# Performance work log

Hardware: AMD Instinct MI355X
Metric: run time of the kernel (lower is better)

Reference implementation:

```python
import jax, jax.numpy as jnp
import numpy as np

N_LOC, N_EVT, E = 100000, 200000, 1000000
F_LOC, F_EVT, H = 128, 128, 64


def setup_inputs() -> dict:
    key = jax.random.key(0)
    ks = jax.random.split(key, 12)
    s = lambda k, shp: jax.random.normal(k, shp, dtype=jnp.float32) * (1.0 / np.sqrt(shp[0]))
    return {
        "loc_x": jax.random.normal(ks[0], (N_LOC, F_LOC), dtype=jnp.float32),
        "evt_x": jax.random.normal(ks[1], (N_EVT, F_EVT), dtype=jnp.float32),
        "edge_index": jax.random.randint(ks[2], (2, E), 0, N_LOC, dtype=jnp.int64),
        # projections (stored as (in, out))
        "W_loc": s(ks[3], (F_LOC, H)), "b_loc": jnp.zeros((H,), jnp.float32),
        "W_evt": s(ks[4], (F_EVT, H)), "b_evt": jnp.zeros((H,), jnp.float32),
        # SAGEConv: lin_l (on aggregated src, with bias), lin_r (on dst root, no bias)
        "W_l": s(ks[5], (H, H)), "b_l": jnp.zeros((H,), jnp.float32),
        "W_r": s(ks[6], (H, H)),
        # head MLP
        "W_h1": s(ks[7], (H, H // 2)), "b_h1": jnp.zeros((H // 2,), jnp.float32),
        "W_h2": s(ks[8], (H // 2, 1)), "b_h2": jnp.zeros((1,), jnp.float32),
    }


def reference(loc_x, evt_x, edge_index, W_loc, b_loc, W_evt, b_evt,
              W_l, b_l, W_r, W_h1, b_h1, W_h2, b_h2):
    # node projections + ReLU
    loc_h = jax.nn.relu(loc_x @ W_loc + b_loc)   # [N_loc, H]
    evt_h = jax.nn.relu(evt_x @ W_evt + b_evt)   # [N_evt, H]

    src, dst = edge_index[0], edge_index[1]      # event -> location
    n_loc = loc_h.shape[0]
    # mean aggregation of source (event) features onto destination (location) nodes
    msg_sum = jax.ops.segment_sum(evt_h[src], dst, num_segments=n_loc)   # [N_loc, H]
    cnt = jax.ops.segment_sum(jnp.ones_like(dst, dtype=loc_h.dtype), dst,
                              num_segments=n_loc)
    agg = msg_sum / jnp.maximum(cnt, 1.0)[:, None]
    # SAGEConv: lin_l(agg) + lin_r(root), then ReLU
    loc_h = jax.nn.relu(agg @ W_l + b_l + loc_h @ W_r)

    # prediction head
    h = jax.nn.relu(loc_h @ W_h1 + b_h1)
    logits = (h @ W_h2 + b_h2)[:, 0]             # [N_loc]
    return logits
```

## Files before the change

### kernel.cpp

```cpp
#include <hip/hip_runtime.h>


#define N_LOC 100000
#define N_EVT 200000
#define E_CNT 1000000
#define NTILES 6250
#define NBKT   256
#define BKT_L  391
#define CAPG   6000
#define QCAP   32
#define BKT_BLK 512
#define PERB   1954

#define PROJ_EVT_BLK 512
#define PROJ_LOC_BLK 256
#define PROJ_BLK_TOT (PROJ_EVT_BLK + PROJ_LOC_BLK)
#define EVT_TILES 12500
#define LOC_TILES 6250
#define HEAD_BLK  512

typedef __attribute__((ext_vector_type(8))) short short8;
typedef __attribute__((ext_vector_type(4))) float floatx4;

__device__ __forceinline__ float b2f(unsigned short u) {
    unsigned int x = ((unsigned int)u) << 16;
    return __builtin_bit_cast(float, x);
}
__device__ __forceinline__ unsigned short f2b(float f) {
    unsigned int x = __builtin_bit_cast(unsigned int, f);
    unsigned int r = (x + 0x7fffu + ((x >> 16) & 1u)) >> 16;
    return (unsigned short)r;
}
__device__ __forceinline__ float loadf(const void* p, int f32, size_t i) {
    return f32 ? ((const float*)p)[i] : b2f(((const unsigned short*)p)[i]);
}

__global__ __launch_bounds__(256) void prep_kernel(
    const void* t0, const void* t1, const int* eidx,
    const void* t3, const void* t4, const void* t5, const void* t6,
    const void* t7, const void* t8, const void* t9, const void* t10,
    const void* t11, const void* t12, const void* t13,
    int* flags, int* gbc, unsigned short* __restrict__ wp_all) {
    int b = blockIdx.x, tid = threadIdx.x;
    __shared__ int s0, s1;

    if (b == 14) { gbc[tid] = 0; return; }

    if (b >= 15) {
        int pb = b - 15;
        const void* W; int K, N, bstart, off;
        if (pb < 4)       { W = t5;  K = 128; N = 64; bstart = 0;  off = 0; }
        else if (pb < 8)  { W = t3;  K = 128; N = 64; bstart = 4;  off = 8192; }
        else if (pb < 10) { W = t7;  K = 64;  N = 64; bstart = 8;  off = 16384; }
        else if (pb < 12) { W = t9;  K = 64;  N = 64; bstart = 10; off = 20480; }
        else              { W = t10; K = 64;  N = 32; bstart = 12; off = 24576; }
        if (tid == 0) s0 = 0;
        __syncthreads();
        int nsamp = 2 * K * N; if (nsamp > 1024) nsamp = 1024;
        const unsigned short* h = (const unsigned short*)W;
        int susp = 0;
        for (int i = tid; i < nsamp; i += 256)
            if (((h[i] >> 7) & 0xFF) >= 0x90) susp++;
        if (susp) atomicAdd(&s0, susp);
        __syncthreads();
        int f32 = (s0 * 16 >= nsamp) ? 1 : 0;

        int idx  = (pb - bstart) * 256 + tid;
        int nk   = K >> 5;
        int f    = idx >> 6;
        int lane = idx & 63;
        int t  = f / nk;
        int kk = f - t * nk;
        int n  = t * 16 + (lane & 15);
        int k0 = kk * 32 + (lane >> 4) * 8;
        unsigned short tmp[8];
#pragma unroll
        for (int j = 0; j < 8; ++j) {
            size_t src = (size_t)(k0 + j) * N + n;
            tmp[j] = f32 ? f2b(((const float*)W)[src])
                         : ((const unsigned short*)W)[src];
        }
#pragma unroll
        for (int j = 0; j < 8; ++j) wp_all[(size_t)off + (size_t)idx * 8 + j] = tmp[j];
        return;
    }

    if (tid == 0) { s0 = 0; s1 = 0; }
    __syncthreads();
    if (b == 13) {
        if (tid < 128) {
            if (eidx[2 * tid] != 0) atomicAdd(&s0, 1);
            if (eidx[2 * tid + 1] != 0) atomicAdd(&s1, 1);
        }
        __syncthreads();
        if (tid == 0) flags[2] = (s1 == 0 && s0 > 32) ? 1 : 0;
        return;
    }
    const void* ptrs[13] = {t0, t1, t3, t4, t5, t6, t7, t8, t9, t10, t11, t12, t13};
    const int   cnts[13] = {12800000, 25600000, 8192, 64, 8192, 64,
                            4096, 64, 4096, 2048, 32, 32, 1};
    const int   slot[13] = {0, 1, 3, 4, 5, 6, 7, 8, 9, 10, 11, 12, 13};
    int nsamp = 2 * cnts[b];
    if (nsamp > 1024) nsamp = 1024;
    const unsigned short* h = (const unsigned short*)ptrs[b];
    int susp = 0;
    for (int i = tid; i < nsamp; i += 256)
        if (((h[i] >> 7) & 0xFF) >= 0x90) susp++;
    if (susp) atomicAdd(&s0, susp);
    __syncthreads();
    if (tid == 0) flags[slot[b]] = (s0 * 16 >= nsamp) ? 1 : 0;
}

__global__ __launch_bounds__(256, 3) void proj_both_kernel(
    const void* __restrict__ evt_x, const void* __restrict__ loc_x,
    const unsigned short* __restrict__ wp_all,
    const void* __restrict__ b_evt, const void* __restrict__ b_loc,
    unsigned short* __restrict__ evt_h, unsigned short* __restrict__ loc_h,
    const int* __restrict__ flags) {
    int blk = blockIdx.x;
    int tid = threadIdx.x, lane = tid & 63, wv = tid >> 6;
    int l15 = lane & 15, quad = lane >> 4;

    const void* X; const unsigned short* Wp; const void* bias;
    unsigned short* Y; int fx, fb, w0, nw, ntile;
    if (blk < PROJ_EVT_BLK) {
        X = evt_x; Wp = wp_all;        bias = b_evt; Y = evt_h;
        fx = flags[1]; fb = flags[6];
        w0 = blk * 4 + wv; nw = PROJ_EVT_BLK * 4; ntile = EVT_TILES;
    } else {
        X = loc_x; Wp = wp_all + 8192; bias = b_loc; Y = loc_h;
        fx = flags[0]; fb = flags[4];
        w0 = (blk - PROJ_EVT_BLK) * 4 + wv; nw = PROJ_LOC_BLK * 4; ntile = LOC_TILES;
    }

    short8 b[16];
#pragma unroll
    for (int f = 0; f < 16; ++f)
        b[f] = *reinterpret_cast<const short8*>(Wp + ((size_t)(f * 64 + lane)) * 8);

    float bv[4];
#pragma unroll
    for (int q = 0; q < 4; ++q) bv[q] = loadf(bias, fb, q * 16 + l15);

    if (w0 >= ntile) return;

    float4 pf[8];
    short8 an[4];

    auto issue = [&](int t) {
        int m = t * 16 + l15;
        if (fx) {
            const float* xr = (const float*)X + (size_t)m * 128 + quad * 8;
#pragma unroll
            for (int kk = 0; kk < 4; ++kk) {
                pf[kk * 2]     = *reinterpret_cast<const float4*>(xr + kk * 32);
                pf[kk * 2 + 1] = *reinterpret_cast<const float4*>(xr + kk * 32 + 4);
            }
        } else {
            const unsigned short* xr = (const unsigned short*)X + (size_t)m * 128 + quad * 8;
#pragma unroll
            for (int kk = 0; kk < 4; ++kk)
                an[kk] = *reinterpret_cast<const short8*>(xr + kk * 32);
        }
    };

    issue(w0);
    for (int t = w0; t < ntile; t += nw) {
        short8 a[4];
        if (fx) {
#pragma unroll
            for (int kk = 0; kk < 4; ++kk) {
                float4 p0 = pf[kk * 2], p1 = pf[kk * 2 + 1];
                short8 v;
                v[0] = (short)f2b(p0.x); v[1] = (short)f2b(p0.y);
                v[2] = (short)f2b(p0.z); v[3] = (short)f2b(p0.w);
                v[4] = (short)f2b(p1.x); v[5] = (short)f2b(p1.y);
                v[6] = (short)f2b(p1.z); v[7] = (short)f2b(p1.w);
                a[kk] = v;
            }
        } else {
#pragma unroll
            for (int kk = 0; kk < 4; ++kk) a[kk] = an[kk];
        }
        int tn = t + nw;
        if (tn < ntile) issue(tn);

        floatx4 acc[4];
#pragma unroll
        for (int q = 0; q < 4; ++q) acc[q] = (floatx4)0.0f;
#pragma unroll
        for (int kk = 0; kk < 4; ++kk)
#pragma unroll
            for (int q = 0; q < 4; ++q)
                acc[q] = __builtin_amdgcn_mfma_f32_16x16x32_bf16(
                    a[kk], b[q * 4 + kk], acc[q], 0, 0, 0);

#pragma unroll
        for (int q = 0; q < 4; ++q)
#pragma unroll
            for (int r = 0; r < 4; ++r) {
                float v = acc[q][r] + bv[q];
                v = v > 0.0f ? v : 0.0f;
                Y[(size_t)(t * 16 + quad * 4 + r) * 64 + q * 16 + l15] = f2b(v);
            }
    }
}

__global__ __launch_bounds__(256) void bucket_kernel(
    const int* __restrict__ eidx, uint2* __restrict__ bkt,
    int* __restrict__ gbc, const int* __restrict__ flags) {
    __shared__ uint2 queue[NBKT][QCAP];
    __shared__ int qcnt[NBKT];
    int tid = threadIdx.x, blk = blockIdx.x;
    qcnt[tid] = 0;
    __syncthreads();
    int f64 = flags[2];
    const long long* e64 = (const long long*)eidx;
    int e0 = blk * PERB;
    int e1 = e0 + PERB; if (e1 > E_CNT) e1 = E_CNT;
    const int rounds = (PERB + 255) / 256;

    for (int r = 0; r < rounds; ++r) {
        int e = e0 + r * 256 + tid;
        if (e < e1) {
            int src, dst;
            if (f64) { src = (int)e64[e]; dst = (int)e64[E_CNT + e]; }
            else     { src = eidx[e];     dst = eidx[E_CNT + e]; }
            if ((unsigned)dst < (unsigned)N_LOC && (unsigned)src < (unsigned)N_EVT) {
                int bk = dst / BKT_L;
                int pos = atomicAdd(&qcnt[bk], 1);
                if (pos < QCAP) {
                    queue[bk][pos] = make_uint2((unsigned)src, (unsigned)dst);
                } else {
                    int p = atomicAdd(&gbc[bk], 1);
                    if (p < CAPG) bkt[(size_t)bk * CAPG + p] = make_uint2(src, dst);
                }
            }
        }
        __syncthreads();
        int n = qcnt[tid]; if (n > QCAP) n = QCAP;
        while (n >= 16) {
            int gp = atomicAdd(&gbc[tid], 16);
            if (gp + 16 <= CAPG) {
                uint2* d = bkt + (size_t)tid * CAPG + gp;
#pragma unroll
                for (int j = 0; j < 16; ++j) d[j] = queue[tid][j];
            }
#pragma unroll
            for (int j = 16; j < QCAP; ++j) queue[tid][j - 16] = queue[tid][j];
            n -= 16;
        }
        qcnt[tid] = n;
        __syncthreads();
    }
    int n = qcnt[tid]; if (n > QCAP) n = QCAP;
    if (n > 0) {
        int gp = atomicAdd(&gbc[tid], n);
        for (int j = 0; j < n; ++j)
            if (gp + j < CAPG) bkt[(size_t)tid * CAPG + gp + j] = queue[tid][j];
    }
}

__global__ void scan_gbc_kernel(const int* __restrict__ gbc,
                                int* __restrict__ bbase) {
    __shared__ int sh[256];
    int t = threadIdx.x;
    int v = gbc[t]; if (v > CAPG) v = CAPG;
    sh[t] = v;
    __syncthreads();
    for (int d = 1; d < 256; d <<= 1) {
        int x = (t >= d) ? sh[t - d] : 0;
        __syncthreads();
        sh[t] += x;
        __syncthreads();
    }
    bbase[t] = sh[t] - v;
}

__global__ __launch_bounds__(256) void csr_build_kernel(
    const uint2* __restrict__ bkt, const int* __restrict__ gbc,
    const int* __restrict__ bbase,
    int* __restrict__ rowptr, int* __restrict__ csr) {
    __shared__ int lcnt[512];
    __shared__ int lscan[512];
    __shared__ int lcsr[CAPG];
    int b = blockIdx.x, tid = threadIdx.x;
    int loc0 = b * BKT_L;
    int nloc = N_LOC - loc0; if (nloc > BKT_L) nloc = BKT_L;
    int cntE = gbc[b]; if (cntE > CAPG) cntE = CAPG;
    int base = bbase[b];
    const uint2* bp = bkt + (size_t)b * CAPG;

    int i0 = tid, i1 = tid + 256;
    lcnt[i0] = 0; lcnt[i1] = 0;
    __syncthreads();
    for (int i = tid; i < cntE; i += 256) {
        int d = (int)bp[i].y - loc0;
        atomicAdd(&lcnt[d], 1);
    }
    __syncthreads();
    lscan[i0] = lcnt[i0]; lscan[i1] = lcnt[i1];
    __syncthreads();
    for (int d = 1; d < 512; d <<= 1) {
        int v0 = (i0 >= d) ? lscan[i0 - d] : 0;
        int v1 = (i1 >= d) ? lscan[i1 - d] : 0;
        __syncthreads();
        lscan[i0] += v0; lscan[i1] += v1;
        __syncthreads();
    }
    for (int i = tid; i < nloc; i += 256) {
        int excl = lscan[i] - lcnt[i];
        rowptr[loc0 + i] = base + excl;
        lcnt[i] = excl;
    }
    if (b == NBKT - 1 && tid == 0) rowptr[N_LOC] = base + cntE;
    __syncthreads();
    for (int i = tid; i < cntE; i += 256) {
        uint2 pr = bp[i];
        int d = (int)pr.y - loc0;
        int p = atomicAdd(&lcnt[d], 1);
        if (p < CAPG) lcsr[p] = (int)pr.x;
    }
    __syncthreads();
    for (int i = tid; i < cntE; i += 256) csr[base + i] = lcsr[i];
}

__global__ __launch_bounds__(256) void aggregate_kernel(
    const unsigned short* __restrict__ evt_h,
    const int* __restrict__ rowptr, const int* __restrict__ csr,
    unsigned short* __restrict__ agg, int N) {
    int wid  = (blockIdx.x * 256 + threadIdx.x) >> 6;
    int lane = threadIdx.x & 63;
    if (wid >= N) return;
    int e0 = rowptr[wid], e1 = rowptr[wid + 1];
    float acc = 0.0f;
    for (int j = e0; j < e1; j += 4) {
        int c1 = j + 1 < e1, c2 = j + 2 < e1, c3 = j + 3 < e1;
        int s0 = csr[j];
        int s1 = csr[c1 ? j + 1 : j];
        int s2 = csr[c2 ? j + 2 : j];
        int s3 = csr[c3 ? j + 3 : j];
        float v0 = b2f(evt_h[(size_t)s0 * 64 + lane]);
        float v1 = b2f(evt_h[(size_t)s1 * 64 + lane]);
        float v2 = b2f(evt_h[(size_t)s2 * 64 + lane]);
        float v3 = b2f(evt_h[(size_t)s3 * 64 + lane]);
        acc += v0;
        if (c1) acc += v1;
        if (c2) acc += v2;
        if (c3) acc += v3;
    }
    float inv = (e1 > e0) ? 1.0f / (float)(e1 - e0) : 0.0f;
    agg[(size_t)wid * 64 + lane] = f2b(acc * inv);
}

__global__ __launch_bounds__(256, 3) void head_kernel(
    const unsigned short* __restrict__ agg,
    const unsigned short* __restrict__ loc_h,
    const unsigned short* __restrict__ wp_all,
    const void* __restrict__ bl, const void* __restrict__ bh1,
    const void* __restrict__ wh2, const void* __restrict__ bh2,
    void* __restrict__ out, const int* __restrict__ flags) {
    __shared__ unsigned short h2s[4][16 * 64];
    int tid = threadIdx.x, lane = tid & 63, wv = tid >> 6;
    int l15 = lane & 15, quad = lane >> 4;
    int fbl = flags[8], fbh1 = flags[11], fwh2 = flags[12], fbh2 = flags[13];
    int fout = flags[0];
    const unsigned short* wp_l  = wp_all + 16384;
    const unsigned short* wp_r  = wp_all + 20480;
    const unsigned short* wp_h1 = wp_all + 24576;

    short8 bwl[8], bwr[8], bw1[4];
#pragma unroll
    for (int f = 0; f < 8; ++f) {
        bwl[f] = *reinterpret_cast<const short8*>(wp_l + ((size_t)(f * 64 + lane)) * 8);
        bwr[f] = *reinterpret_cast<const short8*>(wp_r + ((size_t)(f * 64 + lane)) * 8);
    }
#pragma unroll
    for (int f = 0; f < 4; ++f)
        bw1[f] = *reinterpret_cast<const short8*>(wp_h1 + ((size_t)(f * 64 + lane)) * 8);

    float bbl[4], bh1v[2], w2v[2];
#pragma unroll
    for (int q = 0; q < 4; ++q) bbl[q] = loadf(bl, fbl, q * 16 + l15);
#pragma unroll
    for (int q = 0; q < 2; ++q) {
        bh1v[q] = loadf(bh1, fbh1, q * 16 + l15);
        w2v[q]  = loadf(wh2, fwh2, q * 16 + l15);
    }
    float bb2 = loadf(bh2, fbh2, 0);

    const int NW = HEAD_BLK * 4;
    int w0 = blockIdx.x * 4 + wv;
    if (w0 >= NTILES) return;

    short8 c0[4], c1[4];

    auto issue = [&](short8* c, int t) {
        int m = t * 16 + l15;
#pragma unroll
        for (int kk = 0; kk < 2; ++kk) {
            c[kk]     = *reinterpret_cast<const short8*>(
                agg + (size_t)m * 64 + kk * 32 + quad * 8);
            c[2 + kk] = *reinterpret_cast<const short8*>(
                loc_h + (size_t)m * 64 + kk * 32 + quad * 8);
        }
    };

    auto compute = [&](const short8* c, int tile) {
        floatx4 acc[4];
#pragma unroll
        for (int q = 0; q < 4; ++q) acc[q] = (floatx4)0.0f;
#pragma unroll
        for (int kk = 0; kk < 2; ++kk)
#pragma unroll
            for (int q = 0; q < 4; ++q) {
                acc[q] = __builtin_amdgcn_mfma_f32_16x16x32_bf16(
                    c[kk], bwl[q * 2 + kk], acc[q], 0, 0, 0);
                acc[q] = __builtin_amdgcn_mfma_f32_16x16x32_bf16(
                    c[2 + kk], bwr[q * 2 + kk], acc[q], 0, 0, 0);
            }
#pragma unroll
        for (int q = 0; q < 4; ++q)
#pragma unroll
            for (int r = 0; r < 4; ++r) {
                float v = acc[q][r] + bbl[q];
                v = v > 0.0f ? v : 0.0f;
                h2s[wv][(quad * 4 + r) * 64 + q * 16 + l15] = f2b(v);
            }
        short8 aH[2];
#pragma unroll
        for (int kk = 0; kk < 2; ++kk)
            aH[kk] = *reinterpret_cast<const short8*>(
                &h2s[wv][l15 * 64 + kk * 32 + quad * 8]);

        floatx4 a1[2];
#pragma unroll
        for (int q = 0; q < 2; ++q) a1[q] = (floatx4)0.0f;
#pragma unroll
        for (int kk = 0; kk < 2; ++kk)
#pragma unroll
            for (int q = 0; q < 2; ++q)
                a1[q] = __builtin_amdgcn_mfma_f32_16x16x32_bf16(
                    aH[kk], bw1[q * 2 + kk], a1[q], 0, 0, 0);

        float s[4] = {0.f, 0.f, 0.f, 0.f};
#pragma unroll
        for (int q = 0; q < 2; ++q)
#pragma unroll
            for (int r = 0; r < 4; ++r) {
                float v = a1[q][r] + bh1v[q];
                v = v > 0.0f ? v : 0.0f;
                s[r] += v * w2v[q];
            }
#pragma unroll
        for (int r = 0; r < 4; ++r) {
            s[r] += __shfl_xor(s[r], 1);
            s[r] += __shfl_xor(s[r], 2);
            s[r] += __shfl_xor(s[r], 4);
            s[r] += __shfl_xor(s[r], 8);
        }
#pragma unroll
        for (int r = 0; r < 4; ++r) {
            if (l15 == r) {
                int row = tile * 16 + quad * 4 + r;
                float v = s[r] + bb2;
                if (fout) ((float*)out)[row] = v;
                else      ((unsigned short*)out)[row] = f2b(v);
            }
        }
    };

    issue(c0, w0);
    int t = w0;
    while (true) {
        int tn = t + NW;
        bool hn = tn < NTILES;
        if (hn) issue(c1, tn);
        compute(c0, t);
        if (!hn) break;
        t = tn; tn = t + NW; hn = tn < NTILES;
        if (hn) issue(c0, tn);
        compute(c1, t);
        if (!hn) break;
        t = tn;
    }
}

extern "C" void kernel_launch(void* const* d_in, const int* in_sizes, int n_in,
                              void* d_out, int out_size, void* d_ws, size_t ws_size,
                              hipStream_t stream) {
    (void)in_sizes; (void)n_in; (void)out_size; (void)ws_size;
    const void* loc_x = d_in[0];
    const void* evt_x = d_in[1];
    const int*  eidx  = (const int*)d_in[2];
    const void* W_loc = d_in[3];
    const void* b_loc = d_in[4];
    const void* W_evt = d_in[5];
    const void* b_evt = d_in[6];
    const void* W_l   = d_in[7];
    const void* b_l   = d_in[8];
    const void* W_r   = d_in[9];
    const void* W_h1  = d_in[10];
    const void* b_h1  = d_in[11];
    const void* W_h2  = d_in[12];
    const void* b_h2  = d_in[13];

    char* ws = (char*)d_ws;
    unsigned short* evt_h  = (unsigned short*)(ws);
    unsigned short* loc_h  = (unsigned short*)(ws + 25600000);
    int*            csr    = (int*)(ws + 38400000);
    int*            rowptr = (int*)(ws + 42400000);
    int*            gbc    = (int*)(ws + 42800016);
    int*            bbase  = (int*)(ws + 42801040);
    unsigned short* wp_all = (unsigned short*)(ws + 42802064);
    int*            flags  = (int*)(ws + 42855312);
    uint2*          bkt    = (uint2*)(ws + 42855376);
    unsigned short* agg    = (unsigned short*)(ws + 42855376);

    prep_kernel<<<28, 256, 0, stream>>>(
        loc_x, evt_x, eidx, W_loc, b_loc, W_evt, b_evt,
        W_l, b_l, W_r, W_h1, b_h1, W_h2, b_h2,
        flags, gbc, wp_all);

    proj_both_kernel<<<PROJ_BLK_TOT, 256, 0, stream>>>(
        evt_x, loc_x, wp_all, b_evt, b_loc, evt_h, loc_h, flags);

    bucket_kernel<<<BKT_BLK, 256, 0, stream>>>(eidx, bkt, gbc, flags);
    scan_gbc_kernel<<<1, 256, 0, stream>>>(gbc, bbase);
    csr_build_kernel<<<NBKT, 256, 0, stream>>>(bkt, gbc, bbase, rowptr, csr);

    aggregate_kernel<<<(N_LOC + 3) / 4, 256, 0, stream>>>(evt_h, rowptr, csr,
                                                          agg, N_LOC);

    head_kernel<<<HEAD_BLK, 256, 0, stream>>>(
        agg, loc_h, wp_all, b_l, b_h1, W_h2, b_h2, d_out, flags);
}
```

Before: 321.7 us.

## Stage MFMA weight fragments in shared memory to raise occupancy in proj and head

```diff
diff --git a/kernel.cpp b/kernel.cpp
--- a/kernel.cpp
+++ b/kernel.cpp
@@ -12,8 +12,8 @@
 #define BKT_BLK 512
 #define PERB   1954
 
-#define PROJ_EVT_BLK 512
-#define PROJ_LOC_BLK 256
+#define PROJ_EVT_BLK 1024
+#define PROJ_LOC_BLK 512
 #define PROJ_BLK_TOT (PROJ_EVT_BLK + PROJ_LOC_BLK)
 #define EVT_TILES 12500
 #define LOC_TILES 6250
@@ -111,12 +111,13 @@
     if (tid == 0) flags[slot[b]] = (s0 * 16 >= nsamp) ? 1 : 0;
 }
 
-__global__ __launch_bounds__(256, 3) void proj_both_kernel(
+__global__ __launch_bounds__(256, 4) void proj_both_kernel(
     const void* __restrict__ evt_x, const void* __restrict__ loc_x,
     const unsigned short* __restrict__ wp_all,
     const void* __restrict__ b_evt, const void* __restrict__ b_loc,
     unsigned short* __restrict__ evt_h, unsigned short* __restrict__ loc_h,
     const int* __restrict__ flags) {
+    __shared__ unsigned short bs[8192];
     int blk = blockIdx.x;
     int tid = threadIdx.x, lane = tid & 63, wv = tid >> 6;
     int l15 = lane & 15, quad = lane >> 4;
@@ -133,10 +134,13 @@
         w0 = (blk - PROJ_EVT_BLK) * 4 + wv; nw = PROJ_LOC_BLK * 4; ntile = LOC_TILES;
     }
 
-    short8 b[16];
-#pragma unroll
-    for (int f = 0; f < 16; ++f)
-        b[f] = *reinterpret_cast<const short8*>(Wp + ((size_t)(f * 64 + lane)) * 8);
+    {
+        const short8* src = reinterpret_cast<const short8*>(Wp);
+        short8* dst = reinterpret_cast<short8*>(bs);
+#pragma unroll
+        for (int i = 0; i < 4; ++i) dst[tid + i * 256] = src[tid + i * 256];
+    }
+    __syncthreads();
 
     float bv[4];
 #pragma unroll
@@ -189,11 +193,17 @@
 #pragma unroll
         for (int q = 0; q < 4; ++q) acc[q] = (floatx4)0.0f;
 #pragma unroll
-        for (int kk = 0; kk < 4; ++kk)
-#pragma unroll
-            for (int q = 0; q < 4; ++q)
+        for (int q = 0; q < 4; ++q) {
+            short8 bq[4];
+#pragma unroll
+            for (int kk = 0; kk < 4; ++kk)
+                bq[kk] = *reinterpret_cast<const short8*>(
+                    &bs[((q * 4 + kk) * 64 + lane) * 8]);
+#pragma unroll
+            for (int kk = 0; kk < 4; ++kk)
                 acc[q] = __builtin_amdgcn_mfma_f32_16x16x32_bf16(
-                    a[kk], b[q * 4 + kk], acc[q], 0, 0, 0);
+                    a[kk], bq[kk], acc[q], 0, 0, 0);
+        }
 
 #pragma unroll
         for (int q = 0; q < 4; ++q)
@@ -353,13 +363,16 @@
     agg[(size_t)wid * 64 + lane] = f2b(acc * inv);
 }
 
-__global__ __launch_bounds__(256, 3) void head_kernel(
+__global__ __launch_bounds__(256, 4) void head_kernel(
     const unsigned short* __restrict__ agg,
     const unsigned short* __restrict__ loc_h,
     const unsigned short* __restrict__ wp_all,
     const void* __restrict__ bl, const void* __restrict__ bh1,
     const void* __restrict__ wh2, const void* __restrict__ bh2,
     void* __restrict__ out, const int* __restrict__ flags) {
+    __shared__ unsigned short bls[4096];
+    __shared__ unsigned short brs[4096];
+    __shared__ unsigned short b1s[2048];
     __shared__ unsigned short h2s[4][16 * 64];
     int tid = threadIdx.x, lane = tid & 63, wv = tid >> 6;
     int l15 = lane & 15, quad = lane >> 4;
@@ -369,15 +382,18 @@
     const unsigned short* wp_r  = wp_all + 20480;
     const unsigned short* wp_h1 = wp_all + 24576;
 
-    short8 bwl[8], bwr[8], bw1[4];
-#pragma unroll
-    for (int f = 0; f < 8; ++f) {
-        bwl[f] = *reinterpret_cast<const short8*>(wp_l + ((size_t)(f * 64 + lane)) * 8);
-        bwr[f] = *reinterpret_cast<const short8*>(wp_r + ((size_t)(f * 64 + lane)) * 8);
-    }
-#pragma unroll
-    for (int f = 0; f < 4; ++f)
-        bw1[f] = *reinterpret_cast<const short8*>(wp_h1 + ((size_t)(f * 64 + lane)) * 8);
+    {
+        const short8* sl = reinterpret_cast<const short8*>(wp_l);
+        const short8* sr = reinterpret_cast<const short8*>(wp_r);
+        const short8* s1 = reinterpret_cast<const short8*>(wp_h1);
+        short8* dl = reinterpret_cast<short8*>(bls);
+        short8* dr = reinterpret_cast<short8*>(brs);
+        short8* d1 = reinterpret_cast<short8*>(b1s);
+        dl[tid] = sl[tid]; dl[tid + 256] = sl[tid + 256];
+        dr[tid] = sr[tid]; dr[tid + 256] = sr[tid + 256];
+        d1[tid] = s1[tid];
+    }
+    __syncthreads();
 
     float bbl[4], bh1v[2], w2v[2];
 #pragma unroll
@@ -411,14 +427,23 @@
 #pragma unroll
         for (int q = 0; q < 4; ++q) acc[q] = (floatx4)0.0f;
 #pragma unroll
-        for (int kk = 0; kk < 2; ++kk)
-#pragma unroll
-            for (int q = 0; q < 4; ++q) {
+        for (int q = 0; q < 4; ++q) {
+            short8 bwl[2], bwr[2];
+#pragma unroll
+            for (int kk = 0; kk < 2; ++kk) {
+                bwl[kk] = *reinterpret_cast<const short8*>(
+                    &bls[((q * 2 + kk) * 64 + lane) * 8]);
+                bwr[kk] = *reinterpret_cast<const short8*>(
+                    &brs[((q * 2 + kk) * 64 + lane) * 8]);
+            }
+#pragma unroll
+            for (int kk = 0; kk < 2; ++kk) {
                 acc[q] = __builtin_amdgcn_mfma_f32_16x16x32_bf16(
-                    c[kk], bwl[q * 2 + kk], acc[q], 0, 0, 0);
+                    c[kk], bwl[kk], acc[q], 0, 0, 0);
                 acc[q] = __builtin_amdgcn_mfma_f32_16x16x32_bf16(
-                    c[2 + kk], bwr[q * 2 + kk], acc[q], 0, 0, 0);
-            }
+                    c[2 + kk], bwr[kk], acc[q], 0, 0, 0);
+            }
+        }
 #pragma unroll
         for (int q = 0; q < 4; ++q)
 #pragma unroll
@@ -437,11 +462,17 @@
 #pragma unroll
         for (int q = 0; q < 2; ++q) a1[q] = (floatx4)0.0f;
 #pragma unroll
-        for (int kk = 0; kk < 2; ++kk)
-#pragma unroll
-            for (int q = 0; q < 2; ++q)
+        for (int q = 0; q < 2; ++q) {
+            short8 bw1[2];
+#pragma unroll
+            for (int kk = 0; kk < 2; ++kk)
+                bw1[kk] = *reinterpret_cast<const short8*>(
+                    &b1s[((q * 2 + kk) * 64 + lane) * 8]);
+#pragma unroll
+            for (int kk = 0; kk < 2; ++kk)
                 a1[q] = __builtin_amdgcn_mfma_f32_16x16x32_bf16(
-                    aH[kk], bw1[q * 2 + kk], a1[q], 0, 0, 0);
+                    aH[kk], bw1[kk], a1[q], 0, 0, 0);
+        }
 
         float s[4] = {0.f, 0.f, 0.f, 0.f};
 #pragma unroll
```

New measurement: 347.3 us. 1.08x slower.
